# Performance work log

Hardware: AMD Instinct MI355X
Metric: run time of the kernel (lower is better)

## Reference

```python
import jax, jax.numpy as jnp
import numpy as np

NEARZERO = 1e-5
# Bounds for the 14 parameters consumed by the HBV step, in order:
# BETA, FC, K0, K1, K2, LP, PERC, UZL, TT, CFMAX, CFR, CWH, BETAET, C
BOUNDS = np.array([
    [1.0, 6.0], [50.0, 1000.0], [0.05, 0.9], [0.01, 0.5], [0.001, 0.2],
    [0.2, 1.0], [0.0, 10.0], [0.0, 100.0], [-2.5, 2.5], [0.5, 10.0],
    [0.0, 0.1], [0.0, 0.2], [0.3, 5.0], [0.0, 1.0]], dtype=np.float32)

T, G = 365, 50000


def setup_inputs() -> dict:
    key = jax.random.key(0)
    k1, k2, k3, k4 = jax.random.split(key, 4)
    precip = jax.random.uniform(k1, (T, G), dtype=jnp.float32) * 10.0   # mm/day
    temp = jax.random.normal(k2, (T, G), dtype=jnp.float32) * 10.0      # degC
    pet = jax.random.uniform(k3, (T, G), dtype=jnp.float32) * 5.0       # mm/day
    phy_params = jax.random.uniform(k4, (G, 14), dtype=jnp.float32)     # normalized [0,1]
    return {"precip": precip, "temp": temp, "pet": pet, "phy_params": phy_params}


def _hbv2_scan(precip, temp, pet, phy_params):
    lo = jnp.asarray(BOUNDS[:, 0])
    hi = jnp.asarray(BOUNDS[:, 1])
    p = lo + phy_params * (hi - lo)  # descale, [G, 14]
    (BETA, FC, K0, K1, K2, LP, PERC_p, UZL, TT, CFMAX, CFR, CWH, BETAET, C) = [p[:, i] for i in range(14)]

    def step(state, forc):
        SNOWPACK, MELTWATER, SM, SUZ, SLZ = state
        pr, tm, pe = forc
        is_rain = (tm >= TT).astype(jnp.float32)
        RAIN = pr * is_rain
        SNOW = pr * (1.0 - is_rain)
        SNOWPACK = SNOWPACK + SNOW
        melt = jnp.minimum(jnp.maximum(CFMAX * (tm - TT), 0.0), SNOWPACK)
        MELTWATER = MELTWATER + melt
        SNOWPACK = SNOWPACK - melt
        refreezing = jnp.minimum(jnp.maximum(CFR * CFMAX * (TT - tm), 0.0), MELTWATER)
        SNOWPACK = SNOWPACK + refreezing
        MELTWATER = MELTWATER - refreezing
        tosoil = jnp.maximum(MELTWATER - CWH * SNOWPACK, 0.0)
        MELTWATER = MELTWATER - tosoil
        soil_wetness = jnp.clip((SM / FC) ** BETA, 0.0, 1.0)
        recharge = (RAIN + tosoil) * soil_wetness
        SM = SM + RAIN + tosoil - recharge
        excess = jnp.maximum(SM - FC, 0.0)
        SM = SM - excess
        evapfactor = jnp.clip((SM / (LP * FC)) ** BETAET, 0.0, 1.0)
        ETact = jnp.minimum(SM, pe * evapfactor)
        SM = jnp.maximum(SM - ETact, NEARZERO)
        capillary = jnp.minimum(SLZ, C * SLZ * (1.0 - jnp.minimum(SM / FC, 1.0)))
        SM = jnp.maximum(SM + capillary, NEARZERO)
        SLZ = jnp.maximum(SLZ - capillary, NEARZERO)
        SUZ = SUZ + recharge + excess
        PERC = jnp.minimum(SUZ, PERC_p)
        SUZ = SUZ - PERC
        Q0 = K0 * jnp.maximum(SUZ - UZL, 0.0)
        SUZ = SUZ - Q0
        Q1 = K1 * SUZ
        SUZ = SUZ - Q1
        SLZ = jnp.maximum(SLZ + PERC, 0.0)
        Q2 = K2 * SLZ
        SLZ = SLZ - Q2
        return (SNOWPACK, MELTWATER, SM, SUZ, SLZ), Q0 + Q1 + Q2

    init = tuple(jnp.full((precip.shape[1],), NEARZERO, dtype=jnp.float32) for _ in range(5))
    _, Q = jax.lax.scan(step, init, (precip, temp, pet))
    return Q  # [T, G] total streamflow per timestep per basin


def reference(precip, temp, pet, phy_params):
    return _hbv2_scan(precip, temp, pet, phy_params)
```

## Files before the change

kernel.cpp:

```cpp
#include <hip/hip_runtime.h>

#define NZ 1e-5f
#define TC 16

__device__ __forceinline__ float fast_exp2(float x) {
#if __has_builtin(__builtin_amdgcn_exp2f)
    return __builtin_amdgcn_exp2f(x);
#else
    return exp2f(x);
#endif
}

__device__ __forceinline__ float fast_log2(float x) {
#if __has_builtin(__builtin_amdgcn_logf)
    return __builtin_amdgcn_logf(x);
#else
    return log2f(x);
#endif
}

__device__ __forceinline__ void gload_lds16(const float* src, float* dst_lds) {
    __builtin_amdgcn_global_load_lds(
        (const __attribute__((address_space(1))) void*)src,
        (__attribute__((address_space(3))) void*)dst_lds,
        16, 0, 0);
}

__global__ __launch_bounds__(64, 1) void hbv_kernel(
    const float* __restrict__ precip,
    const float* __restrict__ temp,
    const float* __restrict__ pet,
    const float* __restrict__ phy,
    float* __restrict__ out,
    int G, int T)
{
    __shared__ float lds[2][3][TC][64];

    const int lane = threadIdx.x;
    const int g0   = blockIdx.x * 64;
    const int g    = g0 + lane;
    const bool valid = (g < G);
    const int gp   = valid ? g : (G - 1);

    const float lo[14] = {1.0f, 50.0f, 0.05f, 0.01f, 0.001f, 0.2f, 0.0f,
                          0.0f, -2.5f, 0.5f, 0.0f, 0.0f, 0.3f, 0.0f};
    const float hi[14] = {6.0f, 1000.0f, 0.9f, 0.5f, 0.2f, 1.0f, 10.0f,
                          100.0f, 2.5f, 10.0f, 0.1f, 0.2f, 5.0f, 1.0f};
    float p[14];
#pragma unroll
    for (int i = 0; i < 14; ++i)
        p[i] = lo[i] + phy[gp * 14 + i] * (hi[i] - lo[i]);

    const float BETA = p[0], FC = p[1], K0 = p[2], K1 = p[3], K2 = p[4];
    const float LP = p[5], PERCp = p[6], UZL = p[7], TT = p[8], CFMAX = p[9];
    const float CFR = p[10], CWH = p[11], BETAET = p[12], C = p[13];
    const float invFC   = 1.0f / FC;
    const float invLPFC = 1.0f / (LP * FC);
    const float CFRX    = CFR * CFMAX;
    (void)LP; (void)CFR;

    float SP = NZ, MW = NZ, SM = NZ, SUZ = NZ, SLZ = NZ;

    float swc  = fminf(fast_exp2(BETA * fast_log2(SM * invFC)), 1.0f);
    float CSLZ = C * SLZ;

    auto hbv_step = [&](float pr, float tm, float pe) -> float {
        const float RAIN = (tm >= TT) ? pr : 0.0f;
        const float SNOW = pr - RAIN;
        SP += SNOW;
        float melt = fminf(fmaxf(CFMAX * (tm - TT), 0.0f), SP);
        MW += melt;
        SP -= melt;
        float refr = fminf(fmaxf(CFRX * (TT - tm), 0.0f), MW);
        SP += refr;
        MW -= refr;
        float tosoil = fmaxf(MW - CWH * SP, 0.0f);
        MW -= tosoil;
        float rt = RAIN + tosoil;
        float recharge = rt * swc;
        SM += rt - recharge;
        float excess = fmaxf(SM - FC, 0.0f);
        SM -= excess;
        float ef = fminf(fast_exp2(BETAET * fast_log2(SM * invLPFC)), 1.0f);
        float ETact = fminf(SM, pe * ef);
        SM = fmaxf(SM - ETact, NZ);
        float cap = fminf(SLZ, CSLZ * (1.0f - fminf(SM * invFC, 1.0f)));
        SM = fmaxf(SM + cap, NZ);
        SLZ = fmaxf(SLZ - cap, NZ);
        const float Lnext = fast_log2(SM * invFC);
        SUZ += recharge + excess;
        float PERC = fminf(SUZ, PERCp);
        SUZ -= PERC;
        float Q0 = K0 * fmaxf(SUZ - UZL, 0.0f);
        SUZ -= Q0;
        float Q1 = K1 * SUZ;
        SUZ -= Q1;
        SLZ = fmaxf(SLZ + PERC, 0.0f);
        float Q2 = K2 * SLZ;
        SLZ -= Q2;
        CSLZ = C * SLZ;
        swc  = fminf(fast_exp2(BETA * Lnext), 1.0f);
        return Q0 + Q1 + Q2;
    };

    if ((G & 3) == 0) {
        const int rsub = lane >> 4;
        const int csub = (lane & 15) << 2;
        int gcol = g0 + csub;
        if (gcol > G - 4) gcol = G - 4;

        const int nt = (T + TC - 1) / TC;

        auto issue_tile = [&](int k, int b) {
            const int t0 = k * TC;
#pragma unroll
            for (int q = 0; q < TC / 4; ++q) {
                int t = t0 + 4 * q + rsub;
                if (t > T - 1) t = T - 1;
                const size_t off = (size_t)t * G + gcol;
                gload_lds16(precip + off, &lds[b][0][4 * q][0]);
                gload_lds16(temp   + off, &lds[b][1][4 * q][0]);
                gload_lds16(pet    + off, &lds[b][2][4 * q][0]);
            }
        };

        issue_tile(0, 0);
        asm volatile("s_waitcnt vmcnt(0)" ::: "memory");
        __builtin_amdgcn_sched_barrier(0);

        for (int k = 0; k < nt; ++k) {
            const int b = k & 1;
            if (k + 1 < nt) {
                issue_tile(k + 1, b ^ 1);
                __builtin_amdgcn_sched_barrier(0);
            }
            const int t0 = k * TC;
#pragma unroll
            for (int j = 0; j < TC; ++j) {
                const int t = t0 + j;
                const float pr = lds[b][0][j][lane];
                const float tm = lds[b][1][j][lane];
                const float pe = lds[b][2][j][lane];
                const float q = hbv_step(pr, tm, pe);
                if (valid && t < T)
                    out[(size_t)t * G + g] = q;
            }
            if (k + 1 < nt) {
                asm volatile("s_waitcnt vmcnt(12)" ::: "memory");
                __builtin_amdgcn_sched_barrier(0);
            }
        }
    } else {
        for (int t = 0; t < T; ++t) {
            const size_t idx = (size_t)t * G + gp;
            const float q = hbv_step(precip[idx], temp[idx], pet[idx]);
            if (valid) out[idx] = q;
        }
    }
}

extern "C" void kernel_launch(void* const* d_in, const int* in_sizes, int n_in,
                              void* d_out, int out_size, void* d_ws, size_t ws_size,
                              hipStream_t stream) {
    const float* precip = (const float*)d_in[0];
    const float* temp   = (const float*)d_in[1];
    const float* pet    = (const float*)d_in[2];
    const float* phy    = (const float*)d_in[3];
    float* out = (float*)d_out;

    const int G = in_sizes[3] / 14;
    const int T = in_sizes[0] / G;

    dim3 block(64);
    dim3 grid((G + 63) / 64);
    hbv_kernel<<<grid, block, 0, stream>>>(precip, temp, pet, phy, out, G, T);
}
```

Measured before the change: 255.5 us.

## Replace LDS async tile staging with register double-buffered direct loads

Drops the global-to-LDS async loads and LDS buffers. Each lane now loads its own forcing values straight into two register arrays of 12 timesteps, alternating them so the next tile's loads are in flight while the current tile is computed. The soil-moisture update is also simplified to use fminf and a direct subtraction in place of the separate excess and ETact steps. This removes LDS traffic and the explicit vmcnt waits, but each load is now a scalar per-lane access, register pressure rises, and the path only runs when T/12 is even (true for T=365), with the remaining tail steps handled separately.

```diff
diff --git a/kernel.cpp b/kernel.cpp
--- a/kernel.cpp
+++ b/kernel.cpp
@@ -1,7 +1,7 @@
 #include <hip/hip_runtime.h>
 
 #define NZ 1e-5f
-#define TC 16
+#define TC 12
 
 __device__ __forceinline__ float fast_exp2(float x) {
 #if __has_builtin(__builtin_amdgcn_exp2f)
@@ -19,13 +19,6 @@
 #endif
 }
 
-__device__ __forceinline__ void gload_lds16(const float* src, float* dst_lds) {
-    __builtin_amdgcn_global_load_lds(
-        (const __attribute__((address_space(1))) void*)src,
-        (__attribute__((address_space(3))) void*)dst_lds,
-        16, 0, 0);
-}
-
 __global__ __launch_bounds__(64, 1) void hbv_kernel(
     const float* __restrict__ precip,
     const float* __restrict__ temp,
@@ -34,8 +27,6 @@
     float* __restrict__ out,
     int G, int T)
 {
-    __shared__ float lds[2][3][TC][64];
-
     const int lane = threadIdx.x;
     const int g0   = blockIdx.x * 64;
     const int g    = g0 + lane;
@@ -60,7 +51,6 @@
     (void)LP; (void)CFR;
 
     float SP = NZ, MW = NZ, SM = NZ, SUZ = NZ, SLZ = NZ;
-
     float swc  = fminf(fast_exp2(BETA * fast_log2(SM * invFC)), 1.0f);
     float CSLZ = C * SLZ;
 
@@ -76,80 +66,74 @@
         MW -= refr;
         float tosoil = fmaxf(MW - CWH * SP, 0.0f);
         MW -= tosoil;
-        float rt = RAIN + tosoil;
-        float recharge = rt * swc;
-        SM += rt - recharge;
-        float excess = fmaxf(SM - FC, 0.0f);
-        SM -= excess;
-        float ef = fminf(fast_exp2(BETAET * fast_log2(SM * invLPFC)), 1.0f);
-        float ETact = fminf(SM, pe * ef);
-        SM = fmaxf(SM - ETact, NZ);
-        float cap = fminf(SLZ, CSLZ * (1.0f - fminf(SM * invFC, 1.0f)));
+        const float rt = RAIN + tosoil;
+        const float recharge = rt * swc;
+        const float s_pre = SM + rt - recharge;
+        const float excess = fmaxf(s_pre - FC, 0.0f);
+        SM = fminf(s_pre, FC);
+        const float ef = fminf(fast_exp2(BETAET * fast_log2(SM * invLPFC)), 1.0f);
+        SM = fmaxf(SM - pe * ef, NZ);
+        const float cap = fminf(SLZ, CSLZ * (1.0f - fminf(SM * invFC, 1.0f)));
         SM = fmaxf(SM + cap, NZ);
         SLZ = fmaxf(SLZ - cap, NZ);
         const float Lnext = fast_log2(SM * invFC);
         SUZ += recharge + excess;
-        float PERC = fminf(SUZ, PERCp);
+        const float PERC = fminf(SUZ, PERCp);
         SUZ -= PERC;
-        float Q0 = K0 * fmaxf(SUZ - UZL, 0.0f);
+        const float Q0 = K0 * fmaxf(SUZ - UZL, 0.0f);
         SUZ -= Q0;
-        float Q1 = K1 * SUZ;
+        const float Q1 = K1 * SUZ;
         SUZ -= Q1;
         SLZ = fmaxf(SLZ + PERC, 0.0f);
-        float Q2 = K2 * SLZ;
+        const float Q2 = K2 * SLZ;
         SLZ -= Q2;
         CSLZ = C * SLZ;
         swc  = fminf(fast_exp2(BETA * Lnext), 1.0f);
         return Q0 + Q1 + Q2;
     };
 
-    if ((G & 3) == 0) {
-        const int rsub = lane >> 4;
-        const int csub = (lane & 15) << 2;
-        int gcol = g0 + csub;
-        if (gcol > G - 4) gcol = G - 4;
+    const int nfull = T / TC;
+    const int tail  = T - nfull * TC;
 
-        const int nt = (T + TC - 1) / TC;
+    if (nfull >= 2 && (nfull & 1) == 0) {
+        float prA[TC], tmA[TC], peA[TC], prB[TC], tmB[TC], peB[TC];
 
-        auto issue_tile = [&](int k, int b) {
-            const int t0 = k * TC;
+        auto load_tile = [&](int k, float (&P)[TC], float (&M)[TC], float (&E)[TC]) {
 #pragma unroll
-            for (int q = 0; q < TC / 4; ++q) {
-                int t = t0 + 4 * q + rsub;
+            for (int j = 0; j < TC; ++j) {
+                int t = k * TC + j;
                 if (t > T - 1) t = T - 1;
-                const size_t off = (size_t)t * G + gcol;
-                gload_lds16(precip + off, &lds[b][0][4 * q][0]);
-                gload_lds16(temp   + off, &lds[b][1][4 * q][0]);
-                gload_lds16(pet    + off, &lds[b][2][4 * q][0]);
+                const size_t off = (size_t)t * G + gp;
+                P[j] = precip[off];
+                M[j] = temp[off];
+                E[j] = pet[off];
             }
         };
 
-        issue_tile(0, 0);
-        asm volatile("s_waitcnt vmcnt(0)" ::: "memory");
+        auto compute_tile = [&](const float (&P)[TC], const float (&M)[TC],
+                                const float (&E)[TC], int t0, bool full) {
+#pragma unroll
+            for (int j = 0; j < TC; ++j) {
+                const float q = hbv_step(P[j], M[j], E[j]);
+                if ((full || (t0 + j) < T) && valid)
+                    out[(size_t)(t0 + j) * G + g] = q;
+            }
+        };
+
+        load_tile(0, prA, tmA, peA);
         __builtin_amdgcn_sched_barrier(0);
 
-        for (int k = 0; k < nt; ++k) {
-            const int b = k & 1;
-            if (k + 1 < nt) {
-                issue_tile(k + 1, b ^ 1);
-                __builtin_amdgcn_sched_barrier(0);
-            }
-            const int t0 = k * TC;
-#pragma unroll
-            for (int j = 0; j < TC; ++j) {
-                const int t = t0 + j;
-                const float pr = lds[b][0][j][lane];
-                const float tm = lds[b][1][j][lane];
-                const float pe = lds[b][2][j][lane];
-                const float q = hbv_step(pr, tm, pe);
-                if (valid && t < T)
-                    out[(size_t)t * G + g] = q;
-            }
-            if (k + 1 < nt) {
-                asm volatile("s_waitcnt vmcnt(12)" ::: "memory");
-                __builtin_amdgcn_sched_barrier(0);
-            }
+        for (int k = 0; k < nfull; k += 2) {
+            load_tile(k + 1, prB, tmB, peB);
+            __builtin_amdgcn_sched_barrier(0);
+            compute_tile(prA, tmA, peA, k * TC, true);
+
+            load_tile(k + 2, prA, tmA, peA);
+            __builtin_amdgcn_sched_barrier(0);
+            compute_tile(prB, tmB, peB, (k + 1) * TC, true);
         }
+        if (tail)
+            compute_tile(prA, tmA, peA, nfull * TC, false);
     } else {
         for (int t = 0; t < T; ++t) {
             const size_t idx = (size_t)t * G + gp;
```

New measurement: 251.2 us. Within noise of the previous version (-1.7%).
